# Performance work log

Measured on AMD Instinct MI355X. Metric: run time of the kernel, lower is better.

The kernel has to match this reference:

```python
import jax, jax.numpy as jnp
import numpy as np

B, C, IN_H, IN_W = 32, 16, 64, 64
OUT_H, OUT_W, K, STRIDE = 60, 60, 5, 1


def setup_inputs() -> dict:
    key = jax.random.key(0)
    k1, k2 = jax.random.split(key)
    # spike-like inputs in [0,1)
    in_spikes = jax.random.uniform(k1, (B, C, IN_H, IN_W), dtype=jnp.float32)
    # unshared locally-connected weights: (outH, outW, C_in, K, K, C_out)
    weights = jax.random.normal(k2, (OUT_H, OUT_W, C, K, K, C), dtype=jnp.float32) * (1.0 / (K * K))
    return {"in_spikes": in_spikes, "weights": weights}


def _extract_patches(x, out_h, out_w, k, stride):
    # x: (B, C, H, W) -> patches: (B, C, K, K, out_h, out_w)
    # static K*K loop over kernel offsets (not a data-dim loop)
    rows = []
    for di in range(k):
        cols = []
        for dj in range(k):
            cols.append(x[:, :, di:di + out_h * stride:stride, dj:dj + out_w * stride:stride])
        rows.append(jnp.stack(cols, axis=2))  # (B, C, K, out_h, out_w)
    return jnp.stack(rows, axis=2)  # (B, C, K, K, out_h, out_w)


def reference(in_spikes, weights):
    out_h, out_w, _, k, _, _ = weights.shape
    patches = _extract_patches(in_spikes, out_h, out_w, k, STRIDE)
    # output[b, k_out, i, j] = sum_{c,u,v} patches[b,c,u,v,i,j] * weights[i,j,c,u,v,k_out]
    out = jnp.einsum('bcuvij,ijcuvk->bkij', patches, weights)
    return out
```

## Files before the change

### kernel.cpp

```cpp
#include <hip/hip_runtime.h>
#include <hip/hip_bf16.h>


#define OUT_HW 60
#define IN_HW  64
#define CIN    16
#define COUT   16
#define NPOS   3600
#define BK     512
#define XC_ELE (32u * 64u * 64u * 16u)

typedef __attribute__((ext_vector_type(8))) short bf16x8;
typedef __attribute__((ext_vector_type(4))) float f32x4;

static __device__ __forceinline__ unsigned pk2(float a, float b) {
    union { __hip_bfloat162 h; unsigned u; } cv;
    cv.h = __float22bfloat162_rn(make_float2(a, b));
    return cv.u;
}

static __device__ __forceinline__ void g2lds16(const float* g, float* l) {
    __builtin_amdgcn_global_load_lds(
        (const __attribute__((address_space(1))) unsigned int*)g,
        (__attribute__((address_space(3))) unsigned int*)l, 16, 0, 0);
}

__global__ __launch_bounds__(256)
void make_xc(const float* __restrict__ x, ushort* __restrict__ xc) {
    const int bh = blockIdx.x;
    const int b = bh >> 6, h = bh & 63;
    const int t = threadIdx.x;
    const int cq = t & 3, wc = t >> 2;
    const float* src = x + ((size_t)(b * CIN) * IN_HW + h) * IN_HW + wc;
    float f[4];
#pragma unroll
    for (int e = 0; e < 4; ++e)
        f[e] = src[(size_t)(cq * 4 + e) * (IN_HW * IN_HW)];
    union { ushort4 v; unsigned u[2]; } o;
    o.u[0] = pk2(f[0], f[1]);
    o.u[1] = pk2(f[2], f[3]);
    *(ushort4*)&xc[((size_t)bh * IN_HW + wc) * CIN + cq * 4] = o.v;
}

template<int PACKED>
__global__ __launch_bounds__(128, 3)
void lc_pos(const ushort* __restrict__ xc, const float* __restrict__ w,
            float* __restrict__ dst) {
    __shared__ float sWraw[6400] __attribute__((aligned(16)));

    const int bid = blockIdx.x;
    const int pos = (bid & 7) * 450 + (bid >> 3);
    const int i = pos / OUT_HW, j = pos - i * OUT_HW;
    const int t = threadIdx.x;
    const int lane = t & 63, wv = t >> 6;
    const int l15 = lane & 15, q = lane >> 4;
    const int qh = q >> 1, c0 = (q & 1) << 3;

    const float* wsrc = w + (size_t)pos * 6400 + lane * 4;
    for (int o = wv; o < 25; o += 2)
        g2lds16(wsrc + o * 256, &sWraw[o * 256]);

    const int base_hw = i * IN_HW + j;
    const size_t bofs = (size_t)(wv * 16 + l15) * (IN_HW * IN_HW * CIN);
    bf16x8 xa[13];
#pragma unroll
    for (int cc = 0; cc < 13; ++cc) {
        const int uvB = cc * 2 + qh;
        const int uvA = (uvB < 25) ? uvB : 24;
        const int uA = (uvA * 13) >> 6;
        const int vA = uvA - 5 * uA;
        xa[cc] = *(const bf16x8*)(xc + bofs
                   + (size_t)(base_hw + uA * IN_HW + vA) * CIN + c0);
    }

    __syncthreads();

    f32x4 acc = {0.f, 0.f, 0.f, 0.f};
#pragma unroll
    for (int cc = 0; cc < 13; ++cc) {
        const int uvB = cc * 2 + qh;
        const int okB = (uvB < 25);
        float bfv[8];
#pragma unroll
        for (int jj = 0; jj < 8; ++jj)
            bfv[jj] = okB ? sWraw[(c0 + jj) * 400 + uvB * 16 + l15] : 0.f;
        union { bf16x8 v; unsigned u[4]; } pb;
#pragma unroll
        for (int jj = 0; jj < 4; ++jj) pb.u[jj] = pk2(bfv[2 * jj], bfv[2 * jj + 1]);
        acc = __builtin_amdgcn_mfma_f32_16x16x32_bf16(xa[cc], pb.v, acc, 0, 0, 0);
    }

#pragma unroll
    for (int r = 0; r < 4; ++r) {
        const int o = (wv * 16 + q * 4 + r) * 16 + l15;
        if (PACKED) dst[(size_t)pos * BK + o] = acc[r];
        else        dst[(size_t)o * NPOS + pos] = acc[r];
    }
}

__global__ __launch_bounds__(256)
void transpose_out(const float* __restrict__ src, float* __restrict__ out) {
    __shared__ float tile[64][65];
    const int o0 = blockIdx.x * 64;
    const int k0 = blockIdx.y * 64;
    const int t  = threadIdx.x;
    const int tx = t & 63, ty = t >> 6;
    for (int r = ty; r < 64; r += 4) {
        const int oij = o0 + r;
        if (oij < NPOS) tile[r][tx] = src[(size_t)oij * BK + k0 + tx];
    }
    __syncthreads();
    for (int r = ty; r < 64; r += 4) {
        const int oij = o0 + tx;
        if (oij < NPOS) out[(size_t)(k0 + r) * NPOS + oij] = tile[tx][r];
    }
}

__global__ __launch_bounds__(256)
void lc_naive(const float* __restrict__ x, const float* __restrict__ w,
              float* __restrict__ out) {
    const int gid = blockIdx.x * 256 + threadIdx.x;
    if (gid >= 32 * COUT * NPOS) return;
    const int j = gid % OUT_HW;
    int rest = gid / OUT_HW;
    const int i = rest % OUT_HW; rest /= OUT_HW;
    const int k = rest % COUT;
    const int b = rest / COUT;
    const float* wp = w + (size_t)(i * OUT_HW + j) * 6400 + k;
    float s = 0.f;
    for (int c = 0; c < CIN; ++c)
        for (int u = 0; u < 5; ++u)
            for (int v = 0; v < 5; ++v)
                s += x[((size_t)(b * CIN + c) * IN_HW + i + u) * IN_HW + j + v]
                   * wp[((c * 5 + u) * 5 + v) * COUT];
    out[gid] = s;
}

extern "C" void kernel_launch(void* const* d_in, const int* in_sizes, int n_in,
                              void* d_out, int out_size, void* d_ws, size_t ws_size,
                              hipStream_t stream) {
    const float* x = (const float*)d_in[0];
    const float* w = (const float*)d_in[1];
    float* out = (float*)d_out;

    const size_t xcBytes  = (size_t)XC_ELE * 2;
    const size_t outBytes = (size_t)NPOS * BK * 4;
    ushort* xc = (ushort*)d_ws;

    if (ws_size >= xcBytes + outBytes) {
        float* wsOut = (float*)((char*)d_ws + xcBytes);
        make_xc<<<32 * IN_HW, 256, 0, stream>>>(x, xc);
        lc_pos<1><<<NPOS, 128, 0, stream>>>(xc, w, wsOut);
        transpose_out<<<dim3((NPOS + 63) / 64, BK / 64), 256, 0, stream>>>(wsOut, out);
    } else if (ws_size >= xcBytes) {
        make_xc<<<32 * IN_HW, 256, 0, stream>>>(x, xc);
        lc_pos<0><<<NPOS, 128, 0, stream>>>(xc, w, out);
    } else {
        lc_naive<<<(32 * COUT * NPOS + 255) / 256, 256, 0, stream>>>(x, w, out);
    }
}
```

Baseline: 157.6 us.

## Tile five output columns per block with double-buffered weight loads, drop transpose

Each block now handles five consecutive output positions in a row instead of one. The next position's weights are prefetched into a second LDS buffer while the current one computes. Results are written straight into the final (b,k,i,j) layout, which removes the staging buffer and the separate transpose kernel. The grid shrinks from 3600 to 720 blocks, so there is less parallelism to hide latency, and the strided direct stores may coalesce poorly. LDS use doubles to about 51 KB per block, and the occupancy hint was dropped.

```diff
diff --git a/kernel.cpp b/kernel.cpp
--- a/kernel.cpp
+++ b/kernel.cpp
@@ -7,7 +7,8 @@
 #define CIN    16
 #define COUT   16
 #define NPOS   3600
-#define BK     512
+#define T_J    5
+#define NTILE  720
 #define XC_ELE (32u * 64u * 64u * 16u)
 
 typedef __attribute__((ext_vector_type(8))) short bf16x8;
@@ -42,77 +43,69 @@
     *(ushort4*)&xc[((size_t)bh * IN_HW + wc) * CIN + cq * 4] = o.v;
 }
 
-template<int PACKED>
-__global__ __launch_bounds__(128, 3)
+__global__ __launch_bounds__(128)
 void lc_pos(const ushort* __restrict__ xc, const float* __restrict__ w,
-            float* __restrict__ dst) {
-    __shared__ float sWraw[6400] __attribute__((aligned(16)));
+            float* __restrict__ out) {
+    __shared__ float sW[2][6400] __attribute__((aligned(16)));
 
     const int bid = blockIdx.x;
-    const int pos = (bid & 7) * 450 + (bid >> 3);
-    const int i = pos / OUT_HW, j = pos - i * OUT_HW;
+    const int tt  = (bid & 7) * 90 + (bid >> 3);
+    const int i   = tt / 12, jt = tt - i * 12;
+    const int j0  = jt * T_J;
     const int t = threadIdx.x;
     const int lane = t & 63, wv = t >> 6;
     const int l15 = lane & 15, q = lane >> 4;
     const int qh = q >> 1, c0 = (q & 1) << 3;
 
-    const float* wsrc = w + (size_t)pos * 6400 + lane * 4;
+    const float* wbase = w + (size_t)(i * OUT_HW + j0) * 6400 + lane * 4;
+    const size_t bofs  = (size_t)(wv * 16 + l15) * (IN_HW * IN_HW * CIN);
+
     for (int o = wv; o < 25; o += 2)
-        g2lds16(wsrc + o * 256, &sWraw[o * 256]);
+        g2lds16(wbase + o * 256, &sW[0][o * 256]);
 
-    const int base_hw = i * IN_HW + j;
-    const size_t bofs = (size_t)(wv * 16 + l15) * (IN_HW * IN_HW * CIN);
-    bf16x8 xa[13];
+    for (int p = 0; p < T_J; ++p) {
+        const int base_hw = i * IN_HW + (j0 + p);
+        bf16x8 xa[13];
 #pragma unroll
-    for (int cc = 0; cc < 13; ++cc) {
-        const int uvB = cc * 2 + qh;
-        const int uvA = (uvB < 25) ? uvB : 24;
-        const int uA = (uvA * 13) >> 6;
-        const int vA = uvA - 5 * uA;
-        xa[cc] = *(const bf16x8*)(xc + bofs
-                   + (size_t)(base_hw + uA * IN_HW + vA) * CIN + c0);
-    }
+        for (int cc = 0; cc < 13; ++cc) {
+            const int uvB = cc * 2 + qh;
+            const int uvA = (uvB < 25) ? uvB : 24;
+            const int uA = (uvA * 13) >> 6;
+            const int vA = uvA - 5 * uA;
+            xa[cc] = *(const bf16x8*)(xc + bofs
+                       + (size_t)(base_hw + uA * IN_HW + vA) * CIN + c0);
+        }
 
-    __syncthreads();
+        __syncthreads();
 
-    f32x4 acc = {0.f, 0.f, 0.f, 0.f};
+        if (p + 1 < T_J) {
+            const float* wn = wbase + (size_t)(p + 1) * 6400;
+            float* ld = &sW[(p + 1) & 1][0];
+            for (int o = wv; o < 25; o += 2)
+                g2lds16(wn + o * 256, ld + o * 256);
+        }
+
+        const float* sWb = &sW[p & 1][0];
+        f32x4 acc = {0.f, 0.f, 0.f, 0.f};
 #pragma unroll
-    for (int cc = 0; cc < 13; ++cc) {
-        const int uvB = cc * 2 + qh;
-        const int okB = (uvB < 25);
-        float bfv[8];
+        for (int cc = 0; cc < 13; ++cc) {
+            const int uvB = cc * 2 + qh;
+            const int okB = (uvB < 25);
+            float bfv[8];
 #pragma unroll
-        for (int jj = 0; jj < 8; ++jj)
-            bfv[jj] = okB ? sWraw[(c0 + jj) * 400 + uvB * 16 + l15] : 0.f;
-        union { bf16x8 v; unsigned u[4]; } pb;
+            for (int jj = 0; jj < 8; ++jj)
+                bfv[jj] = okB ? sWb[(c0 + jj) * 400 + uvB * 16 + l15] : 0.f;
+            union { bf16x8 v; unsigned u[4]; } pb;
 #pragma unroll
-        for (int jj = 0; jj < 4; ++jj) pb.u[jj] = pk2(bfv[2 * jj], bfv[2 * jj + 1]);
-        acc = __builtin_amdgcn_mfma_f32_16x16x32_bf16(xa[cc], pb.v, acc, 0, 0, 0);
-    }
+            for (int jj = 0; jj < 4; ++jj) pb.u[jj] = pk2(bfv[2 * jj], bfv[2 * jj + 1]);
+            acc = __builtin_amdgcn_mfma_f32_16x16x32_bf16(xa[cc], pb.v, acc, 0, 0, 0);
+        }
 
 #pragma unroll
-    for (int r = 0; r < 4; ++r) {
-        const int o = (wv * 16 + q * 4 + r) * 16 + l15;
-        if (PACKED) dst[(size_t)pos * BK + o] = acc[r];
-        else        dst[(size_t)o * NPOS + pos] = acc[r];
-    }
-}
-
-__global__ __launch_bounds__(256)
-void transpose_out(const float* __restrict__ src, float* __restrict__ out) {
-    __shared__ float tile[64][65];
-    const int o0 = blockIdx.x * 64;
-    const int k0 = blockIdx.y * 64;
-    const int t  = threadIdx.x;
-    const int tx = t & 63, ty = t >> 6;
-    for (int r = ty; r < 64; r += 4) {
-        const int oij = o0 + r;
-        if (oij < NPOS) tile[r][tx] = src[(size_t)oij * BK + k0 + tx];
-    }
-    __syncthreads();
-    for (int r = ty; r < 64; r += 4) {
-        const int oij = o0 + tx;
-        if (oij < NPOS) out[(size_t)(k0 + r) * NPOS + oij] = tile[tx][r];
+        for (int r = 0; r < 4; ++r) {
+            const int b = wv * 16 + q * 4 + r;
+            out[(size_t)(b * COUT + l15) * NPOS + i * OUT_HW + (j0 + p)] = acc[r];
+        }
     }
 }
 
@@ -143,18 +136,12 @@
     const float* w = (const float*)d_in[1];
     float* out = (float*)d_out;
 
-    const size_t xcBytes  = (size_t)XC_ELE * 2;
-    const size_t outBytes = (size_t)NPOS * BK * 4;
+    const size_t xcBytes = (size_t)XC_ELE * 2;
     ushort* xc = (ushort*)d_ws;
 
-    if (ws_size >= xcBytes + outBytes) {
-        float* wsOut = (float*)((char*)d_ws + xcBytes);
+    if (ws_size >= xcBytes) {
         make_xc<<<32 * IN_HW, 256, 0, stream>>>(x, xc);
-        lc_pos<1><<<NPOS, 128, 0, stream>>>(xc, w, wsOut);
-        transpose_out<<<dim3((NPOS + 63) / 64, BK / 64), 256, 0, stream>>>(wsOut, out);
-    } else if (ws_size >= xcBytes) {
-        make_xc<<<32 * IN_HW, 256, 0, stream>>>(x, xc);
-        lc_pos<0><<<NPOS, 128, 0, stream>>>(xc, w, out);
+        lc_pos<<<NTILE, 128, 0, stream>>>(xc, w, out);
     } else {
         lc_naive<<<(32 * COUT * NPOS + 255) / 256, 256, 0, stream>>>(x, w, out);
     }
```

Measured after the change: 163.0 us. +3.4%, slower.

## Pre-pack weights to bf16 MFMA layout in fused prep kernel, drop LDS staging

Applied to the files above, without the earlier changes.

Adds a prep kernel that converts the per-position fp32 weights into bf16 fragments already laid out for the MFMA B operand, and fuses the input bf16 conversion into the same launch. The main kernel then uses one 64-thread wave per position, loading B fragments straight from global memory and reusing each one for two batch halves, with no LDS staging, barrier or in-loop packing. The cost is an extra full read and write of the weights each call in prep, plus more workspace. If the workspace is too small, execution now falls back to the naive kernel instead of the unpacked MFMA path.

```diff
diff --git a/kernel.cpp b/kernel.cpp
--- a/kernel.cpp
+++ b/kernel.cpp
@@ -8,6 +8,7 @@
 #define COUT   16
 #define NPOS   3600
 #define BK     512
+#define WT_POS 6656
 #define XC_ELE (32u * 64u * 64u * 16u)
 
 typedef __attribute__((ext_vector_type(8))) short bf16x8;
@@ -19,82 +20,82 @@
     return cv.u;
 }
 
-static __device__ __forceinline__ void g2lds16(const float* g, float* l) {
-    __builtin_amdgcn_global_load_lds(
-        (const __attribute__((address_space(1))) unsigned int*)g,
-        (__attribute__((address_space(3))) unsigned int*)l, 16, 0, 0);
+__global__ __launch_bounds__(256)
+void prep(const float* __restrict__ x, const float* __restrict__ w,
+          ushort* __restrict__ xc, ushort* __restrict__ wt) {
+    const int bid = blockIdx.x;
+    const int t = threadIdx.x;
+    if (bid < NPOS) {
+        const float* wbase = w + (size_t)bid * 6400;
+        unsigned* dstd = (unsigned*)(wt + (size_t)bid * WT_POS);
+#pragma unroll
+        for (int it = 0; it < 13; ++it) {
+            const int d = it * 256 + t;
+            const int e = d * 2;
+            const int cc  = e >> 9;
+            const int q   = (e >> 7) & 3;
+            const int l15 = (e >> 3) & 15;
+            const int jj  = e & 7;
+            const int uvB = cc * 2 + (q >> 1);
+            const int c0  = (q & 1) << 3;
+            unsigned val = 0u;
+            if (uvB < 25) {
+                const int m0 = (c0 + jj) * 25 + uvB;
+                val = pk2(wbase[m0 * 16 + l15],
+                          wbase[(m0 + 25) * 16 + l15]);
+            }
+            dstd[d] = val;
+        }
+    } else {
+        const int bh = bid - NPOS;
+        const int b = bh >> 6, h = bh & 63;
+        const int cq = t & 3, wc = t >> 2;
+        const float* src = x + ((size_t)(b * CIN) * IN_HW + h) * IN_HW + wc;
+        float f[4];
+#pragma unroll
+        for (int e = 0; e < 4; ++e)
+            f[e] = src[(size_t)(cq * 4 + e) * (IN_HW * IN_HW)];
+        union { ushort4 v; unsigned u[2]; } o;
+        o.u[0] = pk2(f[0], f[1]);
+        o.u[1] = pk2(f[2], f[3]);
+        *(ushort4*)&xc[((size_t)bh * IN_HW + wc) * CIN + cq * 4] = o.v;
+    }
 }
 
-__global__ __launch_bounds__(256)
-void make_xc(const float* __restrict__ x, ushort* __restrict__ xc) {
-    const int bh = blockIdx.x;
-    const int b = bh >> 6, h = bh & 63;
-    const int t = threadIdx.x;
-    const int cq = t & 3, wc = t >> 2;
-    const float* src = x + ((size_t)(b * CIN) * IN_HW + h) * IN_HW + wc;
-    float f[4];
-#pragma unroll
-    for (int e = 0; e < 4; ++e)
-        f[e] = src[(size_t)(cq * 4 + e) * (IN_HW * IN_HW)];
-    union { ushort4 v; unsigned u[2]; } o;
-    o.u[0] = pk2(f[0], f[1]);
-    o.u[1] = pk2(f[2], f[3]);
-    *(ushort4*)&xc[((size_t)bh * IN_HW + wc) * CIN + cq * 4] = o.v;
-}
-
-template<int PACKED>
-__global__ __launch_bounds__(128, 3)
-void lc_pos(const ushort* __restrict__ xc, const float* __restrict__ w,
-            float* __restrict__ dst) {
-    __shared__ float sWraw[6400] __attribute__((aligned(16)));
-
+__global__ __launch_bounds__(64)
+void lc_main(const ushort* __restrict__ xc, const ushort* __restrict__ wt,
+             float* __restrict__ dst) {
     const int bid = blockIdx.x;
     const int pos = (bid & 7) * 450 + (bid >> 3);
     const int i = pos / OUT_HW, j = pos - i * OUT_HW;
-    const int t = threadIdx.x;
-    const int lane = t & 63, wv = t >> 6;
+    const int lane = threadIdx.x;
     const int l15 = lane & 15, q = lane >> 4;
     const int qh = q >> 1, c0 = (q & 1) << 3;
 
-    const float* wsrc = w + (size_t)pos * 6400 + lane * 4;
-    for (int o = wv; o < 25; o += 2)
-        g2lds16(wsrc + o * 256, &sWraw[o * 256]);
+    const ushort* wtp = wt + (size_t)pos * WT_POS + q * 128 + l15 * 8;
+    const int base_hw = i * IN_HW + j;
+    const size_t bofs0 = (size_t)l15 * (IN_HW * IN_HW * CIN);
+    const size_t bofs1 = (size_t)(l15 + 16) * (IN_HW * IN_HW * CIN);
 
-    const int base_hw = i * IN_HW + j;
-    const size_t bofs = (size_t)(wv * 16 + l15) * (IN_HW * IN_HW * CIN);
-    bf16x8 xa[13];
+    f32x4 acc0 = {0.f, 0.f, 0.f, 0.f}, acc1 = {0.f, 0.f, 0.f, 0.f};
 #pragma unroll
     for (int cc = 0; cc < 13; ++cc) {
         const int uvB = cc * 2 + qh;
         const int uvA = (uvB < 25) ? uvB : 24;
         const int uA = (uvA * 13) >> 6;
         const int vA = uvA - 5 * uA;
-        xa[cc] = *(const bf16x8*)(xc + bofs
-                   + (size_t)(base_hw + uA * IN_HW + vA) * CIN + c0);
-    }
-
-    __syncthreads();
-
-    f32x4 acc = {0.f, 0.f, 0.f, 0.f};
-#pragma unroll
-    for (int cc = 0; cc < 13; ++cc) {
-        const int uvB = cc * 2 + qh;
-        const int okB = (uvB < 25);
-        float bfv[8];
-#pragma unroll
-        for (int jj = 0; jj < 8; ++jj)
-            bfv[jj] = okB ? sWraw[(c0 + jj) * 400 + uvB * 16 + l15] : 0.f;
-        union { bf16x8 v; unsigned u[4]; } pb;
-#pragma unroll
-        for (int jj = 0; jj < 4; ++jj) pb.u[jj] = pk2(bfv[2 * jj], bfv[2 * jj + 1]);
-        acc = __builtin_amdgcn_mfma_f32_16x16x32_bf16(xa[cc], pb.v, acc, 0, 0, 0);
+        const size_t xo = (size_t)(base_hw + uA * IN_HW + vA) * CIN + c0;
+        const bf16x8 bF = *(const bf16x8*)(wtp + cc * 512);
+        const bf16x8 a0 = *(const bf16x8*)(xc + bofs0 + xo);
+        const bf16x8 a1 = *(const bf16x8*)(xc + bofs1 + xo);
+        acc0 = __builtin_amdgcn_mfma_f32_16x16x32_bf16(a0, bF, acc0, 0, 0, 0);
+        acc1 = __builtin_amdgcn_mfma_f32_16x16x32_bf16(a1, bF, acc1, 0, 0, 0);
     }
 
 #pragma unroll
     for (int r = 0; r < 4; ++r) {
-        const int o = (wv * 16 + q * 4 + r) * 16 + l15;
-        if (PACKED) dst[(size_t)pos * BK + o] = acc[r];
-        else        dst[(size_t)o * NPOS + pos] = acc[r];
+        dst[(size_t)pos * BK + (q * 4 + r) * 16 + l15]        = acc0[r];
+        dst[(size_t)pos * BK + (q * 4 + r + 16) * 16 + l15]   = acc1[r];
     }
 }
 
@@ -145,16 +146,15 @@
 
     const size_t xcBytes  = (size_t)XC_ELE * 2;
     const size_t outBytes = (size_t)NPOS * BK * 4;
-    ushort* xc = (ushort*)d_ws;
+    const size_t wtBytes  = (size_t)NPOS * WT_POS * 2;
 
-    if (ws_size >= xcBytes + outBytes) {
-        float* wsOut = (float*)((char*)d_ws + xcBytes);
-        make_xc<<<32 * IN_HW, 256, 0, stream>>>(x, xc);
-        lc_pos<1><<<NPOS, 128, 0, stream>>>(xc, w, wsOut);
+    if (ws_size >= xcBytes + outBytes + wtBytes) {
+        ushort* xc    = (ushort*)d_ws;
+        float*  wsOut = (float*)((char*)d_ws + xcBytes);
+        ushort* wtp   = (ushort*)((char*)d_ws + xcBytes + outBytes);
+        prep<<<NPOS + 2048, 256, 0, stream>>>(x, w, xc, wtp);
+        lc_main<<<NPOS, 64, 0, stream>>>(xc, wtp, wsOut);
         transpose_out<<<dim3((NPOS + 63) / 64, BK / 64), 256, 0, stream>>>(wsOut, out);
-    } else if (ws_size >= xcBytes) {
-        make_xc<<<32 * IN_HW, 256, 0, stream>>>(x, xc);
-        lc_pos<0><<<NPOS, 128, 0, stream>>>(xc, w, out);
     } else {
         lc_naive<<<(32 * COUT * NPOS + 255) / 256, 256, 0, stream>>>(x, w, out);
     }
```

Measured after the change: 173.8 us. 10.2% more time.

## Replace LDS-staged weight loads with direct global loads in single-wave blocks

Applied to the files above, without the earlier changes.

The locally-connected MFMA kernel no longer stages each position's 25.6KB weight tile into shared memory with a block-wide barrier. Each lane now reads its weight values straight from global memory, and a single 64-thread wave computes both batch halves with two accumulators instead of splitting them across two waves. This removes the LDS footprint and the sync, which should allow more resident blocks. In exchange the weight reads are strided, 4-byte scalar global loads (stride 400 floats across jj) rather than 16-byte async copies. The middle fallback path now uses the naive kernel.

```diff
diff --git a/kernel.cpp b/kernel.cpp
--- a/kernel.cpp
+++ b/kernel.cpp
@@ -8,6 +8,7 @@
 #define COUT   16
 #define NPOS   3600
 #define BK     512
+#define BSTR   65536
 #define XC_ELE (32u * 64u * 64u * 16u)
 
 typedef __attribute__((ext_vector_type(8))) short bf16x8;
@@ -17,12 +18,6 @@
     union { __hip_bfloat162 h; unsigned u; } cv;
     cv.h = __float22bfloat162_rn(make_float2(a, b));
     return cv.u;
-}
-
-static __device__ __forceinline__ void g2lds16(const float* g, float* l) {
-    __builtin_amdgcn_global_load_lds(
-        (const __attribute__((address_space(1))) unsigned int*)g,
-        (__attribute__((address_space(3))) unsigned int*)l, 16, 0, 0);
 }
 
 __global__ __launch_bounds__(256)
@@ -42,59 +37,49 @@
     *(ushort4*)&xc[((size_t)bh * IN_HW + wc) * CIN + cq * 4] = o.v;
 }
 
-template<int PACKED>
-__global__ __launch_bounds__(128, 3)
-void lc_pos(const ushort* __restrict__ xc, const float* __restrict__ w,
-            float* __restrict__ dst) {
-    __shared__ float sWraw[6400] __attribute__((aligned(16)));
-
+__global__ __launch_bounds__(64)
+void lc_direct(const ushort* __restrict__ xc, const float* __restrict__ w,
+               float* __restrict__ dst) {
     const int bid = blockIdx.x;
     const int pos = (bid & 7) * 450 + (bid >> 3);
     const int i = pos / OUT_HW, j = pos - i * OUT_HW;
-    const int t = threadIdx.x;
-    const int lane = t & 63, wv = t >> 6;
+    const int lane = threadIdx.x;
     const int l15 = lane & 15, q = lane >> 4;
     const int qh = q >> 1, c0 = (q & 1) << 3;
 
-    const float* wsrc = w + (size_t)pos * 6400 + lane * 4;
-    for (int o = wv; o < 25; o += 2)
-        g2lds16(wsrc + o * 256, &sWraw[o * 256]);
+    const float* wb = w + (size_t)pos * 6400 + (c0 * 25 + qh) * 16 + l15;
+    const int base_hw = i * IN_HW + j;
+    const ushort* xp0 = xc + (size_t)l15 * BSTR;
+    const ushort* xp1 = xp0 + (size_t)16 * BSTR;
 
-    const int base_hw = i * IN_HW + j;
-    const size_t bofs = (size_t)(wv * 16 + l15) * (IN_HW * IN_HW * CIN);
-    bf16x8 xa[13];
+    f32x4 acc0 = {0.f, 0.f, 0.f, 0.f}, acc1 = {0.f, 0.f, 0.f, 0.f};
 #pragma unroll
     for (int cc = 0; cc < 13; ++cc) {
         const int uvB = cc * 2 + qh;
-        const int uvA = (uvB < 25) ? uvB : 24;
+        const bool okB = (uvB < 25);
+        float bf[8];
+#pragma unroll
+        for (int jj = 0; jj < 8; ++jj)
+            bf[jj] = okB ? wb[(jj * 25 + cc * 2) * 16] : 0.f;
+        union { bf16x8 v; unsigned u[4]; } pb;
+#pragma unroll
+        for (int jj = 0; jj < 4; ++jj) pb.u[jj] = pk2(bf[2 * jj], bf[2 * jj + 1]);
+
+        const int uvA = okB ? uvB : 24;
         const int uA = (uvA * 13) >> 6;
         const int vA = uvA - 5 * uA;
-        xa[cc] = *(const bf16x8*)(xc + bofs
-                   + (size_t)(base_hw + uA * IN_HW + vA) * CIN + c0);
-    }
+        const size_t xo = (size_t)(base_hw + uA * IN_HW + vA) * CIN + c0;
+        const bf16x8 a0 = *(const bf16x8*)(xp0 + xo);
+        const bf16x8 a1 = *(const bf16x8*)(xp1 + xo);
 
-    __syncthreads();
-
-    f32x4 acc = {0.f, 0.f, 0.f, 0.f};
-#pragma unroll
-    for (int cc = 0; cc < 13; ++cc) {
-        const int uvB = cc * 2 + qh;
-        const int okB = (uvB < 25);
-        float bfv[8];
-#pragma unroll
-        for (int jj = 0; jj < 8; ++jj)
-            bfv[jj] = okB ? sWraw[(c0 + jj) * 400 + uvB * 16 + l15] : 0.f;
-        union { bf16x8 v; unsigned u[4]; } pb;
-#pragma unroll
-        for (int jj = 0; jj < 4; ++jj) pb.u[jj] = pk2(bfv[2 * jj], bfv[2 * jj + 1]);
-        acc = __builtin_amdgcn_mfma_f32_16x16x32_bf16(xa[cc], pb.v, acc, 0, 0, 0);
+        acc0 = __builtin_amdgcn_mfma_f32_16x16x32_bf16(a0, pb.v, acc0, 0, 0, 0);
+        acc1 = __builtin_amdgcn_mfma_f32_16x16x32_bf16(a1, pb.v, acc1, 0, 0, 0);
     }
 
 #pragma unroll
     for (int r = 0; r < 4; ++r) {
-        const int o = (wv * 16 + q * 4 + r) * 16 + l15;
-        if (PACKED) dst[(size_t)pos * BK + o] = acc[r];
-        else        dst[(size_t)o * NPOS + pos] = acc[r];
+        dst[(size_t)pos * BK + (q * 4 + r) * 16 + l15]      = acc0[r];
+        dst[(size_t)pos * BK + (q * 4 + r + 16) * 16 + l15] = acc1[r];
     }
 }
 
@@ -150,11 +135,11 @@
     if (ws_size >= xcBytes + outBytes) {
         float* wsOut = (float*)((char*)d_ws + xcBytes);
         make_xc<<<32 * IN_HW, 256, 0, stream>>>(x, xc);
-        lc_pos<1><<<NPOS, 128, 0, stream>>>(xc, w, wsOut);
+        lc_direct<<<NPOS, 64, 0, stream>>>(xc, w, wsOut);
         transpose_out<<<dim3((NPOS + 63) / 64, BK / 64), 256, 0, stream>>>(wsOut, out);
     } else if (ws_size >= xcBytes) {
         make_xc<<<32 * IN_HW, 256, 0, stream>>>(x, xc);
-        lc_pos<0><<<NPOS, 128, 0, stream>>>(xc, w, out);
+        lc_naive<<<(32 * COUT * NPOS + 255) / 256, 256, 0, stream>>>(x, w, out);
     } else {
         lc_naive<<<(32 * COUT * NPOS + 255) / 256, 256, 0, stream>>>(x, w, out);
     }
```

Result: slower. 194.0 us (+23.1%).
